# Kernel optimization log

Measured on AMD Instinct MI355X. Metric: run time of the kernel, lower is better.

The kernel has to match this reference:

```python
import jax, jax.numpy as jnp
import numpy as np

B, S, D = 1, 2048, 2048
H, KV, HD = 16, 8, 128
GROUP = H // KV
INTER = 6144
L = 2
VOCAB = 32000
EPS = 1e-6
THETA = 10000.0


def _rope_tables(seq_len, head_dim, theta):
    inv_freq = 1.0 / theta ** (np.arange(0, head_dim, 2, dtype=np.float32) / head_dim)
    pos = np.arange(seq_len, dtype=np.float32)
    ang = pos[:, None] * inv_freq[None, :]
    ang = np.concatenate([ang, ang], axis=1)  # [S, HD]
    return jnp.asarray(np.cos(ang)), jnp.asarray(np.sin(ang))


def setup_inputs() -> dict:
    key = jax.random.key(0)
    ks = jax.random.split(key, 16)
    sd = 0.02
    inp = {}
    inp['input_ids'] = jax.random.randint(ks[0], (B, S), 0, VOCAB, dtype=jnp.int32)
    inp['mask'] = jnp.triu(jnp.ones((S, S), dtype=bool), k=1)  # True = masked (future)
    cos, sin = _rope_tables(S, HD, THETA)
    inp['cos'], inp['sin'] = cos, sin
    inp['embed'] = jax.random.normal(ks[1], (VOCAB, D), jnp.float32) * sd
    # torch Linear convention: weight [out, in], y = x @ W.T
    inp['q_w'] = jax.random.normal(ks[2], (L, H * HD, D), jnp.float32) * sd
    inp['k_w'] = jax.random.normal(ks[3], (L, KV * HD, D), jnp.float32) * sd
    inp['v_w'] = jax.random.normal(ks[4], (L, KV * HD, D), jnp.float32) * sd
    inp['o_w'] = jax.random.normal(ks[5], (L, D, H * HD), jnp.float32) * sd
    inp['qn_scale'] = jnp.ones((L, HD), jnp.float32)
    inp['kn_scale'] = jnp.ones((L, HD), jnp.float32)
    inp['ln1_scale'] = jnp.ones((L, D), jnp.float32)
    inp['ln2_scale'] = jnp.ones((L, D), jnp.float32)
    inp['gate_w'] = jax.random.normal(ks[6], (L, INTER, D), jnp.float32) * sd
    inp['up_w'] = jax.random.normal(ks[7], (L, INTER, D), jnp.float32) * sd
    inp['down_w'] = jax.random.normal(ks[8], (L, D, INTER), jnp.float32) * sd
    return inp


def rms_norm(x, scale, eps=EPS):
    xf = x.astype(jnp.float32)
    var = jnp.mean(xf * xf, axis=-1, keepdims=True)
    return (xf * jax.lax.rsqrt(var + eps) * scale).astype(x.dtype)


def apply_rope(x, cos, sin):
    # x: [B, heads, S, HD]
    s = x.shape[2]
    hd = x.shape[-1]
    x1, x2 = x[..., : hd // 2], x[..., hd // 2:]
    rotated = jnp.concatenate([-x2, x1], axis=-1)
    return x * cos[None, None, :s] + rotated * sin[None, None, :s]


def decoder_layer(h, p, mask, cos, sin):
    (q_w, k_w, v_w, o_w, qn, kn, ln1, ln2, gate_w, up_w, down_w) = p
    b, s, _ = h.shape
    x = rms_norm(h, ln1)
    q = (x @ q_w.T).reshape(b, s, H, HD).transpose(0, 2, 1, 3)   # [B,H,S,HD]
    k = (x @ k_w.T).reshape(b, s, KV, HD).transpose(0, 2, 1, 3)  # [B,KV,S,HD]
    v = (x @ v_w.T).reshape(b, s, KV, HD).transpose(0, 2, 1, 3)
    q = rms_norm(q, qn)
    k = rms_norm(k, kn)
    q = apply_rope(q, cos, sin)
    k = apply_rope(k, cos, sin)
    kr = jnp.repeat(k, GROUP, axis=1)  # GQA head expansion
    vr = jnp.repeat(v, GROUP, axis=1)
    scores = jnp.einsum('bhqd,bhkd->bhqk', q, kr) / jnp.sqrt(jnp.float32(HD))
    scores = jnp.where(mask[None, None], -jnp.inf, scores)
    attn = jax.nn.softmax(scores, axis=-1)
    ctx = jnp.einsum('bhqk,bhkd->bhqd', attn, vr)
    ctx = ctx.transpose(0, 2, 1, 3).reshape(b, s, H * HD)
    h = h + ctx @ o_w.T
    x = rms_norm(h, ln2)
    mlp = (jax.nn.silu(x @ gate_w.T) * (x @ up_w.T)) @ down_w.T
    return h + mlp


def reference(input_ids, mask, cos, sin, embed, q_w, k_w, v_w, o_w,
              qn_scale, kn_scale, ln1_scale, ln2_scale, gate_w, up_w, down_w):
    h = embed[input_ids]  # [B, S, D]
    params = (q_w, k_w, v_w, o_w, qn_scale, kn_scale, ln1_scale, ln2_scale,
              gate_w, up_w, down_w)

    def body(carry, p):
        return decoder_layer(carry, p, mask, cos, sin), None

    h, _ = jax.lax.scan(body, h, params)
    return h
```

## Files before the change

kernel.cpp:

```cpp
#include <hip/hip_runtime.h>
#include <hip/hip_bf16.h>

static constexpr int SEQ   = 2048;
static constexpr int DM    = 2048;
static constexpr int NHEAD = 16;
static constexpr int NKVH  = 8;
static constexpr int HDIM  = 128;
static constexpr int FFN   = 6144;
static constexpr int NLAYER = 2;
static constexpr float EPSV = 1e-6f;
static constexpr int QKVN  = NHEAD * HDIM + 2 * NKVH * HDIM;

typedef __attribute__((ext_vector_type(8))) short bf16x8;
typedef __attribute__((ext_vector_type(4))) float f32x4;

__device__ __forceinline__ float wave_sum(float v) {
#pragma unroll
    for (int o = 32; o > 0; o >>= 1) v += __shfl_xor(v, o);
    return v;
}

__device__ __forceinline__ void gload16(const void* g, void* l) {
    __builtin_amdgcn_global_load_lds(
        (const __attribute__((address_space(1))) void*)g,
        (__attribute__((address_space(3))) void*)l,
        16, 0, 0);
}

__global__ void cvt_bf16_k(const float* __restrict__ in, __hip_bfloat16* __restrict__ out) {
    const long b = ((long)blockIdx.x * 256 + threadIdx.x) * 8;
    const float4 a0 = *(const float4*)(in + b);
    const float4 a1 = *(const float4*)(in + b + 4);
    union { bf16x8 v; __hip_bfloat16 h[8]; } u;
    u.h[0] = __float2bfloat16(a0.x); u.h[1] = __float2bfloat16(a0.y);
    u.h[2] = __float2bfloat16(a0.z); u.h[3] = __float2bfloat16(a0.w);
    u.h[4] = __float2bfloat16(a1.x); u.h[5] = __float2bfloat16(a1.y);
    u.h[6] = __float2bfloat16(a1.z); u.h[7] = __float2bfloat16(a1.w);
    *(bf16x8*)(out + b) = u.v;
}

__global__ void embed_k(const int* __restrict__ ids, const float* __restrict__ emb,
                        float* __restrict__ h) {
    const int s = blockIdx.x;
    const long src = (long)ids[s] * DM;
    for (int t = threadIdx.x; t < DM; t += 256)
        h[(long)s * DM + t] = emb[src + t];
}

__global__ void rmsnorm_k(const float* __restrict__ in, const float* __restrict__ g,
                          __hip_bfloat16* __restrict__ out) {
    const int row = blockIdx.x;
    const float* r = in + (long)row * DM;
    const int tid = threadIdx.x;
    float v[8];
    float ss = 0.f;
#pragma unroll
    for (int t = 0; t < 8; ++t) { v[t] = r[tid + t * 256]; ss += v[t] * v[t]; }
    ss = wave_sum(ss);
    __shared__ float sp[4];
    if ((tid & 63) == 0) sp[tid >> 6] = ss;
    __syncthreads();
    ss = sp[0] + sp[1] + sp[2] + sp[3];
    const float inv = rsqrtf(ss * (1.f / DM) + EPSV);
    __hip_bfloat16* o_ = out + (long)row * DM;
#pragma unroll
    for (int t = 0; t < 8; ++t) {
        const int j = tid + t * 256;
        o_[j] = __float2bfloat16(v[t] * inv * g[j]);
    }
}

__global__ void rmsnorm_res4_k(const float* __restrict__ part, long n,
                               float* __restrict__ h, const float* __restrict__ g,
                               __hip_bfloat16* __restrict__ x) {
    const int row = blockIdx.x;
    const int tid = threadIdx.x;
    float v[8];
    float ss = 0.f;
#pragma unroll
    for (int t = 0; t < 8; ++t) {
        const long idx = (long)row * DM + tid + t * 256;
        float s = h[idx];
#pragma unroll
        for (int z = 0; z < 4; ++z) s += part[(long)z * n + idx];
        h[idx] = s;
        v[t] = s;
        ss += s * s;
    }
    ss = wave_sum(ss);
    __shared__ float sp[4];
    if ((tid & 63) == 0) sp[tid >> 6] = ss;
    __syncthreads();
    ss = sp[0] + sp[1] + sp[2] + sp[3];
    const float inv = rsqrtf(ss * (1.f / DM) + EPSV);
    __hip_bfloat16* o_ = x + (long)row * DM;
#pragma unroll
    for (int t = 0; t < 8; ++t) {
        const int j = tid + t * 256;
        o_[j] = __float2bfloat16(v[t] * inv * g[j]);
    }
}

__global__ void red4res_k(const float* __restrict__ p, long n, float* __restrict__ h) {
    const long i = ((long)blockIdx.x * 256 + threadIdx.x) * 4;
    float4 s = *(const float4*)(h + i);
#pragma unroll
    for (int z = 0; z < 4; ++z) {
        const float4 b = *(const float4*)(p + (long)z * n + i);
        s.x += b.x; s.y += b.y; s.z += b.z; s.w += b.w;
    }
    *(float4*)(h + i) = s;
}

__global__ void qknorm_rope_k(const float* __restrict__ in, long zStride, int inOff,
                              const float* __restrict__ ns,
                              const float* __restrict__ cosT, const float* __restrict__ sinT,
                              __hip_bfloat16* __restrict__ out, int nheads) {
    const int idx = blockIdx.x * 4 + (threadIdx.x >> 6);
    const int lane = threadIdx.x & 63;
    const int s = idx / nheads;
    const int hh = idx - s * nheads;
    const long base = (long)s * QKVN + inOff + hh * HDIM;
    const float x1 = in[base + lane]      + in[zStride + base + lane];
    const float x2 = in[base + lane + 64] + in[zStride + base + lane + 64];
    float ss = wave_sum(x1 * x1 + x2 * x2);
    const float inv = rsqrtf(ss * (1.f / HDIM) + EPSV);
    const float n1 = x1 * inv * ns[lane];
    const float n2 = x2 * inv * ns[lane + 64];
    const float c1 = cosT[s * HDIM + lane],      c2 = cosT[s * HDIM + 64 + lane];
    const float s1 = sinT[s * HDIM + lane],      s2 = sinT[s * HDIM + 64 + lane];
    __hip_bfloat16* w = out + ((long)hh * SEQ + s) * HDIM;
    w[lane]      = __float2bfloat16(n1 * c1 - n2 * s1);
    w[lane + 64] = __float2bfloat16(n2 * c2 + n1 * s2);
}

__global__ void vtrans_k(const float* __restrict__ vf, long zStride, int colOff,
                         __hip_bfloat16* __restrict__ vt) {
    __shared__ float tile[64][65];
    const int s0 = blockIdx.x * 64, d0 = blockIdx.y * 64, kv = blockIdx.z;
    const int lane = threadIdx.x & 63, part = threadIdx.x >> 6;
    for (int r = part; r < 64; r += 4) {
        const long idx = (long)(s0 + r) * QKVN + colOff + kv * HDIM + d0 + lane;
        tile[r][lane] = vf[idx] + vf[zStride + idx];
    }
    __syncthreads();
    for (int r = part; r < 64; r += 4)
        vt[((long)kv * HDIM + d0 + r) * SEQ + s0 + lane] = __float2bfloat16(tile[lane][r]);
}

__global__ void silu_mul_k(__hip_bfloat16* __restrict__ g, const __hip_bfloat16* __restrict__ u) {
    const long i = ((long)blockIdx.x * 256 + threadIdx.x) * 8;
    union { bf16x8 v; __hip_bfloat16 h[8]; } a, b, o;
    a.v = *(const bf16x8*)(g + i);
    b.v = *(const bf16x8*)(u + i);
#pragma unroll
    for (int j = 0; j < 8; ++j) {
        const float xx = __bfloat162float(a.h[j]);
        const float yy = __bfloat162float(b.h[j]);
        const float sv = xx / (1.f + __expf(-xx));
        o.h[j] = __float2bfloat16(sv * yy);
    }
    *(bf16x8*)(g + i) = o.v;
}

__global__ __launch_bounds__(256)
void flash_k(const __hip_bfloat16* __restrict__ qb, const __hip_bfloat16* __restrict__ kb,
             const __hip_bfloat16* __restrict__ vt, __hip_bfloat16* __restrict__ ctx) {
    __shared__ __align__(16) char ks[2][16384];
    __shared__ __align__(16) char vs[2][16384];
    __shared__ __align__(16) char ps[4][2048];

    const int tid = threadIdx.x;
    const int lane = tid & 63;
    const int wid = tid >> 6;
    const int l15 = lane & 15;
    const int l4 = lane >> 4;

    const int x = blockIdx.x;
    const int h = blockIdx.y;
    const int q0 = x * 64;
    const int kvh = h >> 1;
    const int nkt = x + 1;
    const float scale = 0.0883883476483184405f;

    bf16x8 aq[4];
    {
        const __hip_bfloat16* qg = qb + ((long)h * SEQ + q0 + wid * 16 + l15) * HDIM + l4 * 8;
#pragma unroll
        for (int kk = 0; kk < 4; ++kk) aq[kk] = *(const bf16x8*)(qg + kk * 32);
    }

    float mreg[4], lreg[4];
#pragma unroll
    for (int j = 0; j < 4; ++j) { mreg[j] = -3.0e38f; lreg[j] = 0.f; }
    f32x4 oacc[8];
#pragma unroll
    for (int n = 0; n < 8; ++n) oacc[n] = (f32x4){0.f, 0.f, 0.f, 0.f};

    auto stageK = [&](int buf, int kt) {
        const __hip_bfloat16* kg = kb + ((long)kvh * SEQ + kt * 64) * HDIM;
#pragma unroll
        for (int i = 0; i < 4; ++i) {
            const int c = i * 256 + tid;
            const int r = c >> 4, s = c & 15;
            gload16(kg + (long)r * HDIM + ((s ^ (r & 7)) * 8), ks[buf] + c * 16);
        }
    };
    auto stageV = [&](int buf, int kt) {
        const __hip_bfloat16* vg = vt + (long)kvh * HDIM * SEQ + kt * 64;
#pragma unroll
        for (int i = 0; i < 4; ++i) {
            const int c = i * 256 + tid;
            const int r = c >> 3, s = c & 7;
            gload16(vg + (long)r * SEQ + ((s ^ (r & 7)) * 8), vs[buf] + c * 16);
        }
    };

    stageK(0, 0); stageV(0, 0);
    asm volatile("s_waitcnt vmcnt(0)" ::: "memory");
    __builtin_amdgcn_s_barrier();

    for (int kt = 0; kt < nkt; ++kt) {
        const int cur = kt & 1;
        if (kt + 1 < nkt) { stageK(cur ^ 1, kt + 1); stageV(cur ^ 1, kt + 1); }

        f32x4 sac[4];
#pragma unroll
        for (int n = 0; n < 4; ++n) sac[n] = (f32x4){0.f, 0.f, 0.f, 0.f};
#pragma unroll
        for (int kk = 0; kk < 4; ++kk) {
#pragma unroll
            for (int n = 0; n < 4; ++n) {
                const int r = n * 16 + l15;
                const bf16x8 bk = *(const bf16x8*)(ks[cur] + r * 256 + (((kk * 4 + l4) ^ (r & 7)) << 4));
                sac[n] = __builtin_amdgcn_mfma_f32_16x16x32_bf16(aq[kk], bk, sac[n], 0, 0, 0);
            }
        }

        const bool diag = (kt + 1 == nkt);
        float mnj[4], alj[4];
#pragma unroll
        for (int j = 0; j < 4; ++j) {
            float mx = -3.0e38f;
#pragma unroll
            for (int n = 0; n < 4; ++n) {
                float v = sac[n][j] * scale;
                if (diag && (n * 16 + l15 > wid * 16 + l4 * 4 + j)) v = -3.0e38f;
                sac[n][j] = v;
                mx = fmaxf(mx, v);
            }
#pragma unroll
            for (int o = 1; o < 16; o <<= 1) mx = fmaxf(mx, __shfl_xor(mx, o));
            const float mn = fmaxf(mreg[j], mx);
            mnj[j] = mn;
            alj[j] = __expf(mreg[j] - mn);
            mreg[j] = mn;
        }
#pragma unroll
        for (int j = 0; j < 4; ++j) {
            float rs = 0.f;
#pragma unroll
            for (int n = 0; n < 4; ++n) {
                const float e = __expf(sac[n][j] - mnj[j]);
                sac[n][j] = e;
                rs += e;
            }
#pragma unroll
            for (int o = 1; o < 16; o <<= 1) rs += __shfl_xor(rs, o);
            lreg[j] = lreg[j] * alj[j] + rs;
#pragma unroll
            for (int n2 = 0; n2 < 8; ++n2) oacc[n2][j] *= alj[j];
        }

        char* pw = ps[wid];
#pragma unroll
        for (int n = 0; n < 4; ++n)
#pragma unroll
            for (int j = 0; j < 4; ++j) {
                const int r = l4 * 4 + j;
                const int col = n * 16 + l15;
                *(__hip_bfloat16*)(pw + r * 128 + (((col >> 3) ^ (r & 7)) << 4) + (col & 7) * 2) =
                    __float2bfloat16(sac[n][j]);
            }
        asm volatile("s_waitcnt lgkmcnt(0)" ::: "memory");
        __builtin_amdgcn_sched_barrier(0);
#pragma unroll
        for (int kk = 0; kk < 2; ++kk) {
            const bf16x8 ap = *(const bf16x8*)(pw + l15 * 128 + (((kk * 4 + l4) ^ (l15 & 7)) << 4));
#pragma unroll
            for (int n2 = 0; n2 < 8; ++n2) {
                const int r = n2 * 16 + l15;
                const bf16x8 bv = *(const bf16x8*)(vs[cur] + r * 128 + (((kk * 4 + l4) ^ (r & 7)) << 4));
                oacc[n2] = __builtin_amdgcn_mfma_f32_16x16x32_bf16(ap, bv, oacc[n2], 0, 0, 0);
            }
        }

        asm volatile("s_waitcnt vmcnt(0)" ::: "memory");
        __builtin_amdgcn_s_barrier();
    }

#pragma unroll
    for (int j = 0; j < 4; ++j) {
        const float inv = 1.f / lreg[j];
        const long rowb = (long)(q0 + wid * 16 + l4 * 4 + j) * (NHEAD * HDIM) + h * HDIM;
#pragma unroll
        for (int n2 = 0; n2 < 8; ++n2)
            ctx[rowb + n2 * 16 + l15] = __float2bfloat16(oacc[n2][j] * inv);
    }
}

template <int OUT>
__global__ __launch_bounds__(512, 2)
void g8p(const __hip_bfloat16* __restrict__ A, const __hip_bfloat16* __restrict__ B,
         void* __restrict__ Cv, int kLen, int ldA, int ldB, int ldC,
         long bZStride, long cZStride, int kZStride) {
    __shared__ __align__(16) char sA[2][2][16384];
    __shared__ __align__(16) char sB[2][2][16384];

    const int tid = threadIdx.x;
    const int lane = tid & 63;
    const int wid = tid >> 6;
    const int wr = wid >> 2;
    const int wc = wid & 3;
    const int l15 = lane & 15;
    const int l4 = lane >> 4;

    const int row0 = blockIdx.y * 256;
    const int col0 = blockIdx.x * 256;
    const int z = blockIdx.z;
    B += (long)z * bZStride;
    const long cOff = (long)z * cZStride;
    const int k0z = z * kZStride;
    const int nk = kLen / 64;

    f32x4 acc[8][4];
#pragma unroll
    for (int m = 0; m < 8; ++m)
#pragma unroll
        for (int n = 0; n < 4; ++n)
            acc[m][n] = (f32x4){0.f, 0.f, 0.f, 0.f};

    auto stage = [&](int kind, int kt) {
        const int k0 = k0z + kt * 64;
        const __hip_bfloat16* base;
        int ld_;
        char* dst;
        if (kind < 2) { base = A + (long)(row0 + kind * 128) * ldA; ld_ = ldA; dst = sA[kt & 1][kind]; }
        else          { base = B + (long)(col0 + (kind - 2) * 128) * ldB; ld_ = ldB; dst = sB[kt & 1][kind - 2]; }
#pragma unroll
        for (int i = 0; i < 2; ++i) {
            const int c = i * 512 + tid;
            const int r = c >> 3;
            const int s = c & 7;
            gload16(base + (long)r * ld_ + k0 + ((s ^ (r & 7)) * 8), dst + c * 16);
        }
    };

    auto readA = [&](int buf, int p, int mm, int ks) -> bf16x8 {
        const int r = p * 32 + mm * 16 + l15;
        const int q = ks * 4 + l4;
        return *(const bf16x8*)(sA[buf][wr] + r * 128 + ((q ^ (r & 7)) << 4));
    };
    auto readB = [&](int buf, int nn, int ks) -> bf16x8 {
        const int r = (wc & 1) * 64 + nn * 16 + l15;
        const int q = ks * 4 + l4;
        return *(const bf16x8*)(sB[buf][wc >> 1] + r * 128 + ((q ^ (r & 7)) << 4));
    };

    stage(0, 0); stage(1, 0); stage(2, 0); stage(3, 0);
    stage(2, 1); stage(3, 1);
    asm volatile("s_waitcnt vmcnt(4)" ::: "memory");
    __builtin_amdgcn_s_barrier();

    bf16x8 bfrag[4][2];
    for (int t = 0; t < nk; ++t) {
        const int cur = t & 1;
#pragma unroll
        for (int p = 0; p < 4; ++p) {
            bf16x8 a[2][2];
            a[0][0] = readA(cur, p, 0, 0); a[0][1] = readA(cur, p, 0, 1);
            a[1][0] = readA(cur, p, 1, 0); a[1][1] = readA(cur, p, 1, 1);
            if (p == 0) {
#pragma unroll
                for (int n = 0; n < 4; ++n) {
                    bfrag[n][0] = readB(cur, n, 0);
                    bfrag[n][1] = readB(cur, n, 1);
                }
            }
            if (p == 0 && t + 1 < nk) stage(0, t + 1);
            if (p == 1 && t + 1 < nk) stage(1, t + 1);
            if (p == 2 && t + 2 < nk) stage(2, t + 2);
            if (p == 3 && t + 2 < nk) stage(3, t + 2);

            if (p == 0) asm volatile("s_waitcnt lgkmcnt(8)" ::: "memory");
            __builtin_amdgcn_sched_barrier(0);
            if (p == 3) {
                if (t + 2 < nk)      asm volatile("s_waitcnt vmcnt(4)" ::: "memory");
                else if (t + 1 < nk) asm volatile("s_waitcnt vmcnt(0)" ::: "memory");
            }
            __builtin_amdgcn_s_barrier();
            asm volatile("s_waitcnt lgkmcnt(0)" ::: "memory");
            __builtin_amdgcn_sched_barrier(0);

            __builtin_amdgcn_s_setprio(1);
#pragma unroll
            for (int ks = 0; ks < 2; ++ks)
#pragma unroll
                for (int mm = 0; mm < 2; ++mm)
#pragma unroll
                    for (int n = 0; n < 4; ++n)
                        acc[p * 2 + mm][n] = __builtin_amdgcn_mfma_f32_16x16x32_bf16(
                            a[mm][ks], bfrag[n][ks], acc[p * 2 + mm][n], 0, 0, 0);
            __builtin_amdgcn_s_setprio(0);
            __builtin_amdgcn_sched_barrier(0);
            __builtin_amdgcn_s_barrier();
        }
    }

#pragma unroll
    for (int m = 0; m < 8; ++m) {
#pragma unroll
        for (int n = 0; n < 4; ++n) {
            const int rb = row0 + wr * 128 + m * 16 + l4 * 4;
            const int cc = col0 + wc * 64 + n * 16 + l15;
#pragma unroll
            for (int j = 0; j < 4; ++j) {
                const long idx = cOff + (long)(rb + j) * ldC + cc;
                if constexpr (OUT == 0) ((float*)Cv)[idx] = acc[m][n][j];
                else                    ((__hip_bfloat16*)Cv)[idx] = __float2bfloat16(acc[m][n][j]);
            }
        }
    }
}

extern "C" void kernel_launch(void* const* d_in, const int* in_sizes, int n_in,
                              void* d_out, int out_size, void* d_ws, size_t ws_size,
                              hipStream_t stream) {
    const int*   ids  = (const int*)d_in[0];
    const float* cosT = (const float*)d_in[2];
    const float* sinT = (const float*)d_in[3];
    const float* emb  = (const float*)d_in[4];
    const float* q_w  = (const float*)d_in[5];
    const float* k_w  = (const float*)d_in[6];
    const float* v_w  = (const float*)d_in[7];
    const float* o_w  = (const float*)d_in[8];
    const float* qn   = (const float*)d_in[9];
    const float* kn   = (const float*)d_in[10];
    const float* ln1  = (const float*)d_in[11];
    const float* ln2  = (const float*)d_in[12];
    const float* gw   = (const float*)d_in[13];
    const float* uw   = (const float*)d_in[14];
    const float* dw   = (const float*)d_in[15];

    char* W = (char*)d_ws;
    size_t off = 0;
    auto take = [&](size_t nb) { char* p = W + off; off += (nb + 255) & ~(size_t)255; return p; };

    __hip_bfloat16* wqkv = (__hip_bfloat16*) take((size_t)NLAYER * QKVN * DM * 2);
    __hip_bfloat16* wo   = (__hip_bfloat16*) take((size_t)NLAYER * DM * (NHEAD * HDIM) * 2);
    __hip_bfloat16* wgu  = (__hip_bfloat16*) take((size_t)NLAYER * 2 * FFN * DM * 2);
    __hip_bfloat16* wd   = (__hip_bfloat16*) take((size_t)NLAYER * DM * FFN * 2);
    float*          h    = (float*)          take((size_t)SEQ * DM * 4);
    __hip_bfloat16* x    = (__hip_bfloat16*) take((size_t)SEQ * DM * 2);
    float*          part = (float*)          take((size_t)4 * SEQ * DM * 4);
    __hip_bfloat16* qb   = (__hip_bfloat16*) take((size_t)NHEAD * SEQ * HDIM * 2);
    __hip_bfloat16* kb   = (__hip_bfloat16*) take((size_t)NKVH * SEQ * HDIM * 2);
    __hip_bfloat16* vt   = (__hip_bfloat16*) take((size_t)NKVH * HDIM * SEQ * 2);
    __hip_bfloat16* ctx  = (__hip_bfloat16*) take((size_t)SEQ * NHEAD * HDIM * 2);
    __hip_bfloat16* go2  = (__hip_bfloat16*) take((size_t)2 * SEQ * FFN * 2);
    if (off > ws_size) return;

    auto cvt = [&](const float* src, __hip_bfloat16* dst, long n) {
        cvt_bf16_k<<<(int)(n / 2048), 256, 0, stream>>>(src, dst);
    };

    for (int l = 0; l < NLAYER; ++l) {
        __hip_bfloat16* base = wqkv + (size_t)l * QKVN * DM;
        cvt(q_w + (size_t)l * (NHEAD * HDIM) * DM, base,                               (long)(NHEAD * HDIM) * DM);
        cvt(k_w + (size_t)l * (NKVH * HDIM) * DM,  base + (size_t)(NHEAD * HDIM) * DM, (long)(NKVH * HDIM) * DM);
        cvt(v_w + (size_t)l * (NKVH * HDIM) * DM,  base + (size_t)(NHEAD * HDIM + NKVH * HDIM) * DM, (long)(NKVH * HDIM) * DM);
        cvt(gw + (size_t)l * FFN * DM, wgu + (size_t)(2 * l)     * FFN * DM, (long)FFN * DM);
        cvt(uw + (size_t)l * FFN * DM, wgu + (size_t)(2 * l + 1) * FFN * DM, (long)FFN * DM);
    }
    cvt(o_w, wo, (long)NLAYER * DM * (NHEAD * HDIM));
    cvt(dw,  wd, (long)NLAYER * DM * FFN);

    embed_k<<<SEQ, 256, 0, stream>>>(ids, emb, h);
    rmsnorm_k<<<SEQ, 256, 0, stream>>>(h, ln1, x);

    const long nQKV = (long)SEQ * QKVN;
    const long nDM  = (long)SEQ * DM;

    for (int l = 0; l < NLAYER; ++l) {
        g8p<0><<<dim3(QKVN / 256, SEQ / 256, 2), 512, 0, stream>>>(
            x, wqkv + (size_t)l * QKVN * DM, part, DM / 2, DM, DM, QKVN,
            0L, nQKV, DM / 2);

        qknorm_rope_k<<<SEQ * NHEAD / 4, 256, 0, stream>>>(
            part, nQKV, 0, qn + l * HDIM, cosT, sinT, qb, NHEAD);
        qknorm_rope_k<<<SEQ * NKVH / 4, 256, 0, stream>>>(
            part, nQKV, NHEAD * HDIM, kn + l * HDIM, cosT, sinT, kb, NKVH);
        vtrans_k<<<dim3(SEQ / 64, HDIM / 64, NKVH), 256, 0, stream>>>(
            part, nQKV, NHEAD * HDIM + NKVH * HDIM, vt);

        flash_k<<<dim3(32, NHEAD), 256, 0, stream>>>(qb, kb, vt, ctx);

        g8p<0><<<dim3(DM / 256, SEQ / 256, 4), 512, 0, stream>>>(
            ctx, wo + (size_t)l * DM * (NHEAD * HDIM), part, (NHEAD * HDIM) / 4,
            NHEAD * HDIM, NHEAD * HDIM, DM, 0L, nDM, (NHEAD * HDIM) / 4);
        rmsnorm_res4_k<<<SEQ, 256, 0, stream>>>(part, nDM, h, ln2 + l * DM, x);

        g8p<1><<<dim3(FFN / 256, SEQ / 256, 2), 512, 0, stream>>>(
            x, wgu + (size_t)(2 * l) * FFN * DM, go2, DM, DM, DM, FFN,
            (long)FFN * DM, (long)SEQ * FFN, 0);
        silu_mul_k<<<(int)(((long)SEQ * FFN) / 2048), 256, 0, stream>>>(go2, go2 + (size_t)SEQ * FFN);

        g8p<0><<<dim3(DM / 256, SEQ / 256, 4), 512, 0, stream>>>(
            go2, wd + (size_t)l * DM * FFN, part, FFN / 4,
            FFN, FFN, DM, 0L, nDM, FFN / 4);
        if (l + 1 < NLAYER)
            rmsnorm_res4_k<<<SEQ, 256, 0, stream>>>(part, nDM, h, ln1 + (l + 1) * DM, x);
        else
            red4res_k<<<(int)(nDM / 1024), 256, 0, stream>>>(part, nDM, h);
    }

    hipMemcpyAsync(d_out, h, (size_t)out_size * sizeof(float), hipMemcpyDeviceToDevice, stream);
}
```

Baseline: 981.0 us.

## Store split-K partials as bf16, pair causal flash tiles, swizzle GEMM blocks

Switches the split-K partial buffers from fp32 to bf16 by making the GEMMs use the bf16-output template, and updates the reduction, norm and rope consumers to match. This halves partial-sum traffic at the cost of rounding each partial to bf16 before accumulation. Flash attention now processes a short and a long causal query tile per block to balance work, and adds s_setprio around the MFMA loops. GEMM workgroups are also remapped with an XCD-aware swizzle, and the rmsnorm and reduction kernels use vectorized loads.

```diff
diff --git a/kernel.cpp b/kernel.cpp
--- a/kernel.cpp
+++ b/kernel.cpp
@@ -70,49 +70,60 @@
     }
 }
 
-__global__ void rmsnorm_res4_k(const float* __restrict__ part, long n,
+__global__ void rmsnorm_res4_k(const __hip_bfloat16* __restrict__ part, long n,
                                float* __restrict__ h, const float* __restrict__ g,
                                __hip_bfloat16* __restrict__ x) {
     const int row = blockIdx.x;
     const int tid = threadIdx.x;
+    const long base = (long)row * DM + tid * 8;
     float v[8];
+    *(float4*)&v[0] = *(const float4*)(h + base);
+    *(float4*)&v[4] = *(const float4*)(h + base + 4);
+#pragma unroll
+    for (int z = 0; z < 4; ++z) {
+        union { bf16x8 vv; __hip_bfloat16 e[8]; } p;
+        p.vv = *(const bf16x8*)(part + (long)z * n + base);
+#pragma unroll
+        for (int j = 0; j < 8; ++j) v[j] += __bfloat162float(p.e[j]);
+    }
+    *(float4*)(h + base) = *(float4*)&v[0];
+    *(float4*)(h + base + 4) = *(float4*)&v[4];
     float ss = 0.f;
 #pragma unroll
-    for (int t = 0; t < 8; ++t) {
-        const long idx = (long)row * DM + tid + t * 256;
-        float s = h[idx];
-#pragma unroll
-        for (int z = 0; z < 4; ++z) s += part[(long)z * n + idx];
-        h[idx] = s;
-        v[t] = s;
-        ss += s * s;
-    }
+    for (int j = 0; j < 8; ++j) ss += v[j] * v[j];
     ss = wave_sum(ss);
     __shared__ float sp[4];
     if ((tid & 63) == 0) sp[tid >> 6] = ss;
     __syncthreads();
     ss = sp[0] + sp[1] + sp[2] + sp[3];
     const float inv = rsqrtf(ss * (1.f / DM) + EPSV);
-    __hip_bfloat16* o_ = x + (long)row * DM;
-#pragma unroll
-    for (int t = 0; t < 8; ++t) {
-        const int j = tid + t * 256;
-        o_[j] = __float2bfloat16(v[t] * inv * g[j]);
-    }
-}
-
-__global__ void red4res_k(const float* __restrict__ p, long n, float* __restrict__ h) {
-    const long i = ((long)blockIdx.x * 256 + threadIdx.x) * 4;
-    float4 s = *(const float4*)(h + i);
+    const float4 g0 = *(const float4*)(g + tid * 8);
+    const float4 g1 = *(const float4*)(g + tid * 8 + 4);
+    union { bf16x8 vv; __hip_bfloat16 e[8]; } o;
+    o.e[0] = __float2bfloat16(v[0] * inv * g0.x); o.e[1] = __float2bfloat16(v[1] * inv * g0.y);
+    o.e[2] = __float2bfloat16(v[2] * inv * g0.z); o.e[3] = __float2bfloat16(v[3] * inv * g0.w);
+    o.e[4] = __float2bfloat16(v[4] * inv * g1.x); o.e[5] = __float2bfloat16(v[5] * inv * g1.y);
+    o.e[6] = __float2bfloat16(v[6] * inv * g1.z); o.e[7] = __float2bfloat16(v[7] * inv * g1.w);
+    *(bf16x8*)(x + base) = o.vv;
+}
+
+__global__ void red4res_k(const __hip_bfloat16* __restrict__ p, long n, float* __restrict__ h) {
+    const long i = ((long)blockIdx.x * 256 + threadIdx.x) * 8;
+    float v[8];
+    *(float4*)&v[0] = *(const float4*)(h + i);
+    *(float4*)&v[4] = *(const float4*)(h + i + 4);
 #pragma unroll
     for (int z = 0; z < 4; ++z) {
-        const float4 b = *(const float4*)(p + (long)z * n + i);
-        s.x += b.x; s.y += b.y; s.z += b.z; s.w += b.w;
-    }
-    *(float4*)(h + i) = s;
-}
-
-__global__ void qknorm_rope_k(const float* __restrict__ in, long zStride, int inOff,
+        union { bf16x8 vv; __hip_bfloat16 e[8]; } b;
+        b.vv = *(const bf16x8*)(p + (long)z * n + i);
+#pragma unroll
+        for (int j = 0; j < 8; ++j) v[j] += __bfloat162float(b.e[j]);
+    }
+    *(float4*)(h + i) = *(float4*)&v[0];
+    *(float4*)(h + i + 4) = *(float4*)&v[4];
+}
+
+__global__ void qknorm_rope_k(const __hip_bfloat16* __restrict__ in, long zStride, int inOff,
                               const float* __restrict__ ns,
                               const float* __restrict__ cosT, const float* __restrict__ sinT,
                               __hip_bfloat16* __restrict__ out, int nheads) {
@@ -121,8 +132,8 @@
     const int s = idx / nheads;
     const int hh = idx - s * nheads;
     const long base = (long)s * QKVN + inOff + hh * HDIM;
-    const float x1 = in[base + lane]      + in[zStride + base + lane];
-    const float x2 = in[base + lane + 64] + in[zStride + base + lane + 64];
+    const float x1 = __bfloat162float(in[base + lane]) + __bfloat162float(in[zStride + base + lane]);
+    const float x2 = __bfloat162float(in[base + lane + 64]) + __bfloat162float(in[zStride + base + lane + 64]);
     float ss = wave_sum(x1 * x1 + x2 * x2);
     const float inv = rsqrtf(ss * (1.f / HDIM) + EPSV);
     const float n1 = x1 * inv * ns[lane];
@@ -134,14 +145,14 @@
     w[lane + 64] = __float2bfloat16(n2 * c2 + n1 * s2);
 }
 
-__global__ void vtrans_k(const float* __restrict__ vf, long zStride, int colOff,
+__global__ void vtrans_k(const __hip_bfloat16* __restrict__ vf, long zStride, int colOff,
                          __hip_bfloat16* __restrict__ vt) {
     __shared__ float tile[64][65];
     const int s0 = blockIdx.x * 64, d0 = blockIdx.y * 64, kv = blockIdx.z;
     const int lane = threadIdx.x & 63, part = threadIdx.x >> 6;
     for (int r = part; r < 64; r += 4) {
         const long idx = (long)(s0 + r) * QKVN + colOff + kv * HDIM + d0 + lane;
-        tile[r][lane] = vf[idx] + vf[zStride + idx];
+        tile[r][lane] = __bfloat162float(vf[idx]) + __bfloat162float(vf[zStride + idx]);
     }
     __syncthreads();
     for (int r = part; r < 64; r += 4)
@@ -176,26 +187,9 @@
     const int l15 = lane & 15;
     const int l4 = lane >> 4;
 
-    const int x = blockIdx.x;
     const int h = blockIdx.y;
-    const int q0 = x * 64;
     const int kvh = h >> 1;
-    const int nkt = x + 1;
     const float scale = 0.0883883476483184405f;
-
-    bf16x8 aq[4];
-    {
-        const __hip_bfloat16* qg = qb + ((long)h * SEQ + q0 + wid * 16 + l15) * HDIM + l4 * 8;
-#pragma unroll
-        for (int kk = 0; kk < 4; ++kk) aq[kk] = *(const bf16x8*)(qg + kk * 32);
-    }
-
-    float mreg[4], lreg[4];
-#pragma unroll
-    for (int j = 0; j < 4; ++j) { mreg[j] = -3.0e38f; lreg[j] = 0.f; }
-    f32x4 oacc[8];
-#pragma unroll
-    for (int n = 0; n < 8; ++n) oacc[n] = (f32x4){0.f, 0.f, 0.f, 0.f};
 
     auto stageK = [&](int buf, int kt) {
         const __hip_bfloat16* kg = kb + ((long)kvh * SEQ + kt * 64) * HDIM;
@@ -216,96 +210,121 @@
         }
     };
 
-    stageK(0, 0); stageV(0, 0);
-    asm volatile("s_waitcnt vmcnt(0)" ::: "memory");
-    __builtin_amdgcn_s_barrier();
-
-    for (int kt = 0; kt < nkt; ++kt) {
-        const int cur = kt & 1;
-        if (kt + 1 < nkt) { stageK(cur ^ 1, kt + 1); stageV(cur ^ 1, kt + 1); }
-
-        f32x4 sac[4];
-#pragma unroll
-        for (int n = 0; n < 4; ++n) sac[n] = (f32x4){0.f, 0.f, 0.f, 0.f};
-#pragma unroll
-        for (int kk = 0; kk < 4; ++kk) {
-#pragma unroll
-            for (int n = 0; n < 4; ++n) {
-                const int r = n * 16 + l15;
-                const bf16x8 bk = *(const bf16x8*)(ks[cur] + r * 256 + (((kk * 4 + l4) ^ (r & 7)) << 4));
-                sac[n] = __builtin_amdgcn_mfma_f32_16x16x32_bf16(aq[kk], bk, sac[n], 0, 0, 0);
-            }
-        }
-
-        const bool diag = (kt + 1 == nkt);
-        float mnj[4], alj[4];
-#pragma unroll
-        for (int j = 0; j < 4; ++j) {
-            float mx = -3.0e38f;
-#pragma unroll
-            for (int n = 0; n < 4; ++n) {
-                float v = sac[n][j] * scale;
-                if (diag && (n * 16 + l15 > wid * 16 + l4 * 4 + j)) v = -3.0e38f;
-                sac[n][j] = v;
-                mx = fmaxf(mx, v);
-            }
-#pragma unroll
-            for (int o = 1; o < 16; o <<= 1) mx = fmaxf(mx, __shfl_xor(mx, o));
-            const float mn = fmaxf(mreg[j], mx);
-            mnj[j] = mn;
-            alj[j] = __expf(mreg[j] - mn);
-            mreg[j] = mn;
-        }
-#pragma unroll
-        for (int j = 0; j < 4; ++j) {
-            float rs = 0.f;
-#pragma unroll
-            for (int n = 0; n < 4; ++n) {
-                const float e = __expf(sac[n][j] - mnj[j]);
-                sac[n][j] = e;
-                rs += e;
-            }
-#pragma unroll
-            for (int o = 1; o < 16; o <<= 1) rs += __shfl_xor(rs, o);
-            lreg[j] = lreg[j] * alj[j] + rs;
-#pragma unroll
-            for (int n2 = 0; n2 < 8; ++n2) oacc[n2][j] *= alj[j];
-        }
-
-        char* pw = ps[wid];
-#pragma unroll
-        for (int n = 0; n < 4; ++n)
-#pragma unroll
-            for (int j = 0; j < 4; ++j) {
-                const int r = l4 * 4 + j;
-                const int col = n * 16 + l15;
-                *(__hip_bfloat16*)(pw + r * 128 + (((col >> 3) ^ (r & 7)) << 4) + (col & 7) * 2) =
-                    __float2bfloat16(sac[n][j]);
-            }
-        asm volatile("s_waitcnt lgkmcnt(0)" ::: "memory");
-        __builtin_amdgcn_sched_barrier(0);
-#pragma unroll
-        for (int kk = 0; kk < 2; ++kk) {
-            const bf16x8 ap = *(const bf16x8*)(pw + l15 * 128 + (((kk * 4 + l4) ^ (l15 & 7)) << 4));
-#pragma unroll
-            for (int n2 = 0; n2 < 8; ++n2) {
-                const int r = n2 * 16 + l15;
-                const bf16x8 bv = *(const bf16x8*)(vs[cur] + r * 128 + (((kk * 4 + l4) ^ (r & 7)) << 4));
-                oacc[n2] = __builtin_amdgcn_mfma_f32_16x16x32_bf16(ap, bv, oacc[n2], 0, 0, 0);
-            }
-        }
-
+#pragma unroll
+    for (int half = 0; half < 2; ++half) {
+        const int x = half ? 31 - blockIdx.x : blockIdx.x;
+        const int q0 = x * 64;
+        const int nkt = x + 1;
+
+        bf16x8 aq[4];
+        {
+            const __hip_bfloat16* qg = qb + ((long)h * SEQ + q0 + wid * 16 + l15) * HDIM + l4 * 8;
+#pragma unroll
+            for (int kk = 0; kk < 4; ++kk) aq[kk] = *(const bf16x8*)(qg + kk * 32);
+        }
+
+        float mreg[4], lreg[4];
+#pragma unroll
+        for (int j = 0; j < 4; ++j) { mreg[j] = -3.0e38f; lreg[j] = 0.f; }
+        f32x4 oacc[8];
+#pragma unroll
+        for (int n = 0; n < 8; ++n) oacc[n] = (f32x4){0.f, 0.f, 0.f, 0.f};
+
+        stageK(0, 0); stageV(0, 0);
         asm volatile("s_waitcnt vmcnt(0)" ::: "memory");
         __builtin_amdgcn_s_barrier();
-    }
-
-#pragma unroll
-    for (int j = 0; j < 4; ++j) {
-        const float inv = 1.f / lreg[j];
-        const long rowb = (long)(q0 + wid * 16 + l4 * 4 + j) * (NHEAD * HDIM) + h * HDIM;
-#pragma unroll
-        for (int n2 = 0; n2 < 8; ++n2)
-            ctx[rowb + n2 * 16 + l15] = __float2bfloat16(oacc[n2][j] * inv);
+
+        for (int kt = 0; kt < nkt; ++kt) {
+            const int cur = kt & 1;
+            if (kt + 1 < nkt) { stageK(cur ^ 1, kt + 1); stageV(cur ^ 1, kt + 1); }
+
+            f32x4 sac[4];
+#pragma unroll
+            for (int n = 0; n < 4; ++n) sac[n] = (f32x4){0.f, 0.f, 0.f, 0.f};
+            __builtin_amdgcn_s_setprio(1);
+#pragma unroll
+            for (int kk = 0; kk < 4; ++kk) {
+#pragma unroll
+                for (int n = 0; n < 4; ++n) {
+                    const int r = n * 16 + l15;
+                    const bf16x8 bk = *(const bf16x8*)(ks[cur] + r * 256 + (((kk * 4 + l4) ^ (r & 7)) << 4));
+                    sac[n] = __builtin_amdgcn_mfma_f32_16x16x32_bf16(aq[kk], bk, sac[n], 0, 0, 0);
+                }
+            }
+            __builtin_amdgcn_s_setprio(0);
+
+            const bool diag = (kt + 1 == nkt);
+            float mnj[4], alj[4];
+#pragma unroll
+            for (int j = 0; j < 4; ++j) {
+                float mx = -3.0e38f;
+#pragma unroll
+                for (int n = 0; n < 4; ++n) {
+                    float v = sac[n][j] * scale;
+                    if (diag && (n * 16 + l15 > wid * 16 + l4 * 4 + j)) v = -3.0e38f;
+                    sac[n][j] = v;
+                    mx = fmaxf(mx, v);
+                }
+#pragma unroll
+                for (int o = 1; o < 16; o <<= 1) mx = fmaxf(mx, __shfl_xor(mx, o));
+                const float mn = fmaxf(mreg[j], mx);
+                mnj[j] = mn;
+                alj[j] = __expf(mreg[j] - mn);
+                mreg[j] = mn;
+            }
+#pragma unroll
+            for (int j = 0; j < 4; ++j) {
+                float rs = 0.f;
+#pragma unroll
+                for (int n = 0; n < 4; ++n) {
+                    const float e = __expf(sac[n][j] - mnj[j]);
+                    sac[n][j] = e;
+                    rs += e;
+                }
+#pragma unroll
+                for (int o = 1; o < 16; o <<= 1) rs += __shfl_xor(rs, o);
+                lreg[j] = lreg[j] * alj[j] + rs;
+#pragma unroll
+                for (int n2 = 0; n2 < 8; ++n2) oacc[n2][j] *= alj[j];
+            }
+
+            char* pw = ps[wid];
+#pragma unroll
+            for (int n = 0; n < 4; ++n)
+#pragma unroll
+                for (int j = 0; j < 4; ++j) {
+                    const int r = l4 * 4 + j;
+                    const int col = n * 16 + l15;
+                    *(__hip_bfloat16*)(pw + r * 128 + (((col >> 3) ^ (r & 7)) << 4) + (col & 7) * 2) =
+                        __float2bfloat16(sac[n][j]);
+                }
+            asm volatile("s_waitcnt lgkmcnt(0)" ::: "memory");
+            __builtin_amdgcn_sched_barrier(0);
+            __builtin_amdgcn_s_setprio(1);
+#pragma unroll
+            for (int kk = 0; kk < 2; ++kk) {
+                const bf16x8 ap = *(const bf16x8*)(pw + l15 * 128 + (((kk * 4 + l4) ^ (l15 & 7)) << 4));
+#pragma unroll
+                for (int n2 = 0; n2 < 8; ++n2) {
+                    const int r = n2 * 16 + l15;
+                    const bf16x8 bv = *(const bf16x8*)(vs[cur] + r * 128 + (((kk * 4 + l4) ^ (r & 7)) << 4));
+                    oacc[n2] = __builtin_amdgcn_mfma_f32_16x16x32_bf16(ap, bv, oacc[n2], 0, 0, 0);
+                }
+            }
+            __builtin_amdgcn_s_setprio(0);
+
+            asm volatile("s_waitcnt vmcnt(0)" ::: "memory");
+            __builtin_amdgcn_s_barrier();
+        }
+
+#pragma unroll
+        for (int j = 0; j < 4; ++j) {
+            const float inv = 1.f / lreg[j];
+            const long rowb = (long)(q0 + wid * 16 + l4 * 4 + j) * (NHEAD * HDIM) + h * HDIM;
+#pragma unroll
+            for (int n2 = 0; n2 < 8; ++n2)
+                ctx[rowb + n2 * 16 + l15] = __float2bfloat16(oacc[n2][j] * inv);
+        }
     }
 }
 
@@ -325,8 +344,14 @@
     const int l15 = lane & 15;
     const int l4 = lane >> 4;
 
-    const int row0 = blockIdx.y * 256;
-    const int col0 = blockIdx.x * 256;
+    const int gx = gridDim.x;
+    const int nwg = gx * gridDim.y;
+    const int lin = blockIdx.y * gx + blockIdx.x;
+    const int cpx = nwg >> 3;
+    const int swz = (lin & 7) * cpx + (lin >> 3);
+    const int row0 = (swz / gx) * 256;
+    const int col0 = (swz % gx) * 256;
+
     const int z = blockIdx.z;
     B += (long)z * bZStride;
     const long cOff = (long)z * cZStride;
@@ -462,7 +487,7 @@
     __hip_bfloat16* wd   = (__hip_bfloat16*) take((size_t)NLAYER * DM * FFN * 2);
     float*          h    = (float*)          take((size_t)SEQ * DM * 4);
     __hip_bfloat16* x    = (__hip_bfloat16*) take((size_t)SEQ * DM * 2);
-    float*          part = (float*)          take((size_t)4 * SEQ * DM * 4);
+    __hip_bfloat16* part = (__hip_bfloat16*) take((size_t)4 * SEQ * DM * 2);
     __hip_bfloat16* qb   = (__hip_bfloat16*) take((size_t)NHEAD * SEQ * HDIM * 2);
     __hip_bfloat16* kb   = (__hip_bfloat16*) take((size_t)NKVH * SEQ * HDIM * 2);
     __hip_bfloat16* vt   = (__hip_bfloat16*) take((size_t)NKVH * HDIM * SEQ * 2);
@@ -492,7 +517,7 @@
     const long nDM  = (long)SEQ * DM;
 
     for (int l = 0; l < NLAYER; ++l) {
-        g8p<0><<<dim3(QKVN / 256, SEQ / 256, 2), 512, 0, stream>>>(
+        g8p<1><<<dim3(QKVN / 256, SEQ / 256, 2), 512, 0, stream>>>(
             x, wqkv + (size_t)l * QKVN * DM, part, DM / 2, DM, DM, QKVN,
             0L, nQKV, DM / 2);
 
@@ -503,9 +528,9 @@
         vtrans_k<<<dim3(SEQ / 64, HDIM / 64, NKVH), 256, 0, stream>>>(
             part, nQKV, NHEAD * HDIM + NKVH * HDIM, vt);
 
-        flash_k<<<dim3(32, NHEAD), 256, 0, stream>>>(qb, kb, vt, ctx);
-
-        g8p<0><<<dim3(DM / 256, SEQ / 256, 4), 512, 0, stream>>>(
+        flash_k<<<dim3(16, NHEAD), 256, 0, stream>>>(qb, kb, vt, ctx);
+
+        g8p<1><<<dim3(DM / 256, SEQ / 256, 4), 512, 0, stream>>>(
             ctx, wo + (size_t)l * DM * (NHEAD * HDIM), part, (NHEAD * HDIM) / 4,
             NHEAD * HDIM, NHEAD * HDIM, DM, 0L, nDM, (NHEAD * HDIM) / 4);
         rmsnorm_res4_k<<<SEQ, 256, 0, stream>>>(part, nDM, h, ln2 + l * DM, x);
@@ -515,13 +540,13 @@
             (long)FFN * DM, (long)SEQ * FFN, 0);
         silu_mul_k<<<(int)(((long)SEQ * FFN) / 2048), 256, 0, stream>>>(go2, go2 + (size_t)SEQ * FFN);
 
-        g8p<0><<<dim3(DM / 256, SEQ / 256, 4), 512, 0, stream>>>(
+        g8p<1><<<dim3(DM / 256, SEQ / 256, 4), 512, 0, stream>>>(
             go2, wd + (size_t)l * DM * FFN, part, FFN / 4,
             FFN, FFN, DM, 0L, nDM, FFN / 4);
         if (l + 1 < NLAYER)
             rmsnorm_res4_k<<<SEQ, 256, 0, stream>>>(part, nDM, h, ln1 + (l + 1) * DM, x);
         else
-            red4res_k<<<(int)(nDM / 1024), 256, 0, stream>>>(part, nDM, h);
+            red4res_k<<<(int)(nDM / 2048), 256, 0, stream>>>(part, nDM, h);
     }
 
     hipMemcpyAsync(d_out, h, (size_t)out_size * sizeof(float), hipMemcpyDeviceToDevice, stream);
```

Result: no change. 965.7 us (-1.6%).
